# Optimization experiments

Measured on AMD Instinct MI355X. Metric: run time of the kernel, lower is better.

The kernel has to match this reference:

```python
import jax, jax.numpy as jnp
import numpy as np
import math

B, L, D = 8, 2048, 256
NUM_TYPES = 1
T_MAX = 200.0
SIGMA = 1.0


def setup_inputs() -> dict:
    key = jax.random.key(0)
    ks = jax.random.split(key, 12)
    event_type = jnp.ones((B, L), dtype=jnp.int64 if jax.config.jax_enable_x64 else jnp.int32)
    t = jax.random.uniform(ks[0], (B, L), dtype=jnp.float32) * T_MAX
    event_time = jnp.sort(t, axis=-1)
    s = 1.0 / math.sqrt(D)
    emb_weight = jax.random.normal(ks[1], (NUM_TYPES + 1, D), jnp.float32)
    emb_weight = emb_weight.at[0].set(0.0)  # padding_idx=0
    gate_w = jax.random.normal(ks[2], (2, D), jnp.float32) * s
    gate_b = jnp.zeros((2,), jnp.float32)
    ker_w = jax.random.normal(ks[3], (1, D), jnp.float32) * s
    ker_b = jnp.zeros((1,), jnp.float32)
    ln_gamma = jnp.ones((D,), jnp.float32)
    ln_beta = jnp.zeros((D,), jnp.float32)
    gen_input_w = jax.random.normal(ks[4], (D, D), jnp.float32) * s
    gen_noise_w = jax.random.normal(ks[5], (D, D), jnp.float32) * s
    gen_out_w = jax.random.normal(ks[6], (1, D), jnp.float32) * s
    gen_out_b = jnp.zeros((1,), jnp.float32)
    noise = jax.random.uniform(ks[7], (B, L, D), jnp.float32)  # torch.rand noise in Generator
    return dict(event_type=event_type, event_time=event_time, emb_weight=emb_weight,
                gate_w=gate_w, gate_b=gate_b, ker_w=ker_w, ker_b=ker_b,
                ln_gamma=ln_gamma, ln_beta=ln_beta, gen_input_w=gen_input_w,
                gen_noise_w=gen_noise_w, gen_out_w=gen_out_w, gen_out_b=gen_out_b,
                noise=noise)


def _softplus_beta(x, beta):
    return jax.nn.softplus(beta * x) / beta


def reference(event_type, event_time, emb_weight, gate_w, gate_b, ker_w, ker_b,
              ln_gamma, ln_beta, gen_input_w, gen_noise_w, gen_out_w, gen_out_b, noise):
    d_model = emb_weight.shape[-1]
    # ---- temporal positional encoding (this is `embedding`) ----
    pos_vec = jnp.power(10000.0, 2.0 * jnp.arange(d_model, dtype=jnp.float32) / d_model)
    t = event_time[:, :, None] / pos_vec                      # [B,L,D]
    idx = jnp.arange(d_model)
    temp_enc = jnp.where(idx % 2 == 0, jnp.sin(t), jnp.cos(t))
    # ---- type embedding ----
    te = emb_weight[event_type] * math.sqrt(d_model)          # [B,L,D]
    # ---- pairwise |t_i - t_j| ; xt[b,i,j]=t_i, xt_bar[b,i,j]=t_j ----
    dt = jnp.abs(event_time[:, :, None] - event_time[:, None, :])  # [B,L,L]
    # ---- squared exponential kernel: params depend only on row i (xd[b,i,j]=te[b,i]) ----
    ls = _softplus_beta(te @ ker_w.T + ker_b, 0.2)[..., 0]    # [B,L]
    scores_k = (SIGMA ** 2) * jnp.exp(-(dt ** 2) / (ls[:, :, None] ** 2))
    # ---- sigmoid gate ----
    p = jax.nn.sigmoid(te @ gate_w.T + gate_b)                # [B,L,2]
    l = p[..., 0][:, :, None]
    s = p[..., 1][:, :, None]
    gate = 1.0 + 0.5 * jnp.tanh((dt / T_MAX - l) / s)
    scores = scores_k * gate                                  # [B,L,L]
    # ---- causal mask: strictly-upper-triangle -> -1e10, then softmax ----
    causal = jnp.tril(jnp.ones((event_time.shape[1], event_time.shape[1]), jnp.bool_))
    scores = jnp.where(causal[None], scores, -1e10)
    attn = jax.nn.softmax(scores, axis=-1)
    # ---- hidden = attn @ temp_enc, layernorm ----
    hidden = jnp.einsum('bij,bjd->bid', attn, temp_enc)
    mu = hidden.mean(-1, keepdims=True)
    var = hidden.var(-1, keepdims=True)
    hidden = (hidden - mu) / jnp.sqrt(var + 1e-6) * ln_gamma + ln_beta
    # ---- Generator (dropout in eval = identity) ----
    h = jax.nn.relu(noise @ gen_noise_w.T + hidden @ gen_input_w.T)
    out = jax.nn.softplus(h @ gen_out_w.T + gen_out_b)[..., 0]  # [B,L]
    return out
```

## Files before the change

### kernel.cpp

```cpp
#include <hip/hip_runtime.h>
#include <hip/hip_bf16.h>

#define BD 8
#define LD 2048
#define DD 256

typedef unsigned short ushort_t;
typedef __attribute__((ext_vector_type(8))) short short8;
typedef __attribute__((ext_vector_type(4))) float floatx4;

__device__ __forceinline__ ushort_t f2bfu(float x) {
  __hip_bfloat16 h = __float2bfloat16(x);
  return *reinterpret_cast<ushort_t*>(&h);
}

__device__ __forceinline__ void dma16(const ushort_t* g, ushort_t* l) {
  __builtin_amdgcn_global_load_lds(
      (const __attribute__((address_space(1))) unsigned int*)g,
      (__attribute__((address_space(3))) unsigned int*)l,
      16, 0, 0);
}

__device__ __forceinline__ float sin_acc(float a) {
  float k = rintf(a * 0.15915494f);
  float r = __builtin_fmaf(-k, 6.2831855f, a);
  r = __builtin_fmaf(-k, -1.7484555e-7f, r);
  return __sinf(r);
}
__device__ __forceinline__ float cos_acc(float a) {
  float k = rintf(a * 0.15915494f);
  float r = __builtin_fmaf(-k, 6.2831855f, a);
  r = __builtin_fmaf(-k, -1.7484555e-7f, r);
  return __cosf(r);
}

__global__ __launch_bounds__(256) void k_dots(
    const float* __restrict__ embw, const float* __restrict__ gatew,
    const float* __restrict__ gateb, const float* __restrict__ kerw,
    const float* __restrict__ kerb, float* __restrict__ ptable)
{
  int d = threadIdx.x;
  int lane = d & 63, wvi = d >> 6;
  __shared__ float red[4][3];
  for (int ty = 0; ty < 2; ++ty) {
    float te = embw[ty * DD + d] * 16.0f;
    float p1 = te * kerw[d];
    float p2 = te * gatew[d];
    float p3 = te * gatew[DD + d];
    #pragma unroll
    for (int off = 32; off > 0; off >>= 1) {
      p1 += __shfl_xor(p1, off);
      p2 += __shfl_xor(p2, off);
      p3 += __shfl_xor(p3, off);
    }
    if (lane == 0) { red[wvi][0] = p1; red[wvi][1] = p2; red[wvi][2] = p3; }
    __syncthreads();
    if (d == 0) {
      float s1 = red[0][0] + red[1][0] + red[2][0] + red[3][0] + kerb[0];
      float s2 = red[0][1] + red[1][1] + red[2][1] + red[3][1] + gateb[0];
      float s3 = red[0][2] + red[1][2] + red[2][2] + red[3][2] + gateb[1];
      float z = 0.2f * s1;
      float sp = (z > 15.0f) ? z : log1pf(__expf(z));
      float ls = 5.0f * sp;
      ptable[ty * 4 + 0] = 1.0f / (ls * ls);
      ptable[ty * 4 + 1] = 1.0f / (1.0f + __expf(-s2));
      float s = 1.0f / (1.0f + __expf(-s3));
      ptable[ty * 4 + 2] = 1.0f / s;
    }
    __syncthreads();
  }
}

__global__ __launch_bounds__(256) void k_prep_enc(
    const float* __restrict__ etime, ushort_t* __restrict__ enc_bf)
{
  int bk = blockIdx.x;
  int tid = threadIdx.x;
  __shared__ float ts[32];
  if (tid < 32) ts[tid] = etime[(bk >> 6) * LD + (bk & 63) * 32 + tid];
  __syncthreads();
  uint4* dst = (uint4*)(enc_bf + (size_t)bk * 8192);
  const int jb = (tid & 3) * 8;
  #pragma unroll
  for (int jblk = 0; jblk < 4; ++jblk) {
    int d = jblk * 64 + (tid >> 2);
    float freq = __expf(-0.07195578416f * (float)d);
    unsigned int pk[4];
    #pragma unroll
    for (int p = 0; p < 4; ++p) {
      float a0 = ts[jb + 2 * p] * freq;
      float a1 = ts[jb + 2 * p + 1] * freq;
      float v0 = (d & 1) ? cos_acc(a0) : sin_acc(a0);
      float v1 = (d & 1) ? cos_acc(a1) : sin_acc(a1);
      pk[p] = (unsigned int)f2bfu(v0) | ((unsigned int)f2bfu(v1) << 16);
    }
    dst[jblk * 256 + tid] = make_uint4(pk[0], pk[1], pk[2], pk[3]);
  }
}

__global__ __launch_bounds__(256) void k_cast(
    const float* __restrict__ noise, const float* __restrict__ wn,
    const float* __restrict__ wi, ushort_t* __restrict__ noise_bf,
    ushort_t* __restrict__ wcat)
{
  int idx = blockIdx.x * 256 + threadIdx.x;
  if (idx < 1048576) {
    float4 f = ((const float4*)noise)[idx];
    ushort4 u;
    u.x = f2bfu(f.x); u.y = f2bfu(f.y); u.z = f2bfu(f.z); u.w = f2bfu(f.w);
    *(ushort4*)(noise_bf + (size_t)idx * 4) = u;
  } else {
    int p = idx - 1048576;
    int c = p >> 7;
    int k = (p & 127) * 4;
    const float* src = (k < 256) ? (wn + c * 256 + k) : (wi + c * 256 + (k - 256));
    float4 f = *(const float4*)src;
    ushort4 u;
    u.x = f2bfu(f.x); u.y = f2bfu(f.y); u.z = f2bfu(f.z); u.w = f2bfu(f.w);
    *(ushort4*)(wcat + (size_t)c * 512 + k) = u;
  }
}

__global__ __launch_bounds__(256, 4) void k_attn(
    const ushort_t* __restrict__ enc_bf, const float* __restrict__ etime,
    const int* __restrict__ etype, const float* __restrict__ ptable,
    const float* __restrict__ gamma, const float* __restrict__ beta,
    ushort_t* __restrict__ hidden_bf)
{
  __shared__ __align__(16) ushort_t stage[4][8192];
  const int tid = threadIdx.x;
  const int lane = tid & 63, wv = tid >> 6;
  const int bk = blockIdx.x;
  const int b = bk & 7;
  const int tl = 127 - (bk >> 3);
  const int base = b * LD;
  const int m = lane & 15, kg = lane >> 4;
  const int i = tl * 16 + m;
  const float ti = etime[base + i];
  const int ty = etype[base + i];
  const float il = ptable[ty * 4 + 0];
  const float ll = ptable[ty * 4 + 1];
  const float is2 = 2.0f * ptable[ty * 4 + 2];
  floatx4 acc[16];
  #pragma unroll
  for (int nt = 0; nt < 16; ++nt) acc[nt] = (floatx4){0.f, 0.f, 0.f, 0.f};
  const int nch = tl / 2 + 1;
  const ushort_t* __restrict__ encC = enc_bf + (size_t)(b * 64) * 8192;
  const int boff = m * 32 + kg * 8;
  ushort_t* mybuf = &stage[wv][0];
  for (int ch = wv; ch < nch; ch += 4) {
    const int j0 = ch * 32 + kg * 8;
    float4 tja = *(const float4*)(etime + base + j0);
    float4 tjb = *(const float4*)(etime + base + j0 + 4);
    __builtin_amdgcn_s_waitcnt(0xC07F);
    const ushort_t* gsrc = encC + (size_t)ch * 8192 + lane * 8;
    #pragma unroll
    for (int nt = 0; nt < 16; ++nt)
      dma16(gsrc + nt * 512, mybuf + nt * 512);
    float tj[8] = {tja.x, tja.y, tja.z, tja.w, tjb.x, tjb.y, tjb.z, tjb.w};
    short8 af;
    #pragma unroll
    for (int v = 0; v < 8; ++v) {
      float dt = fabsf(ti - tj[v]);
      float sk = __expf(-dt * dt * il);
      float rg = __builtin_amdgcn_rcpf(__expf((dt * 0.005f - ll) * is2) + 1.0f);
      float w = __expf(sk * (1.5f - rg));
      w = (j0 + v <= i) ? w : 0.0f;
      af[v] = (short)f2bfu(w);
    }
    __builtin_amdgcn_s_waitcnt(0x0F70);
    #pragma unroll
    for (int nt = 0; nt < 16; ++nt) {
      short8 bf = *(const short8*)(mybuf + nt * 512 + boff);
      acc[nt] = __builtin_amdgcn_mfma_f32_16x16x32_bf16(af, bf, acc[nt], 0, 0, 0);
    }
  }
  __syncthreads();
  floatx4* lds_acc = (floatx4*)&stage[0][0];
  if (wv != 0) {
    #pragma unroll
    for (int nt = 0; nt < 16; ++nt) lds_acc[(nt * 3 + (wv - 1)) * 64 + lane] = acc[nt];
  }
  __syncthreads();
  if (wv == 0) {
    #pragma unroll
    for (int nt = 0; nt < 16; ++nt) {
      acc[nt] += lds_acc[(nt * 3 + 0) * 64 + lane];
      acc[nt] += lds_acc[(nt * 3 + 1) * 64 + lane];
      acc[nt] += lds_acc[(nt * 3 + 2) * 64 + lane];
    }
    float gl[16], cl[16];
    #pragma unroll
    for (int nt = 0; nt < 16; ++nt) { gl[nt] = gamma[nt * 16 + m]; cl[nt] = beta[nt * 16 + m]; }
    const int q = lane >> 4;
    #pragma unroll
    for (int r = 0; r < 4; ++r) {
      float h[16];
      float sm = 0.0f, sq = 0.0f;
      #pragma unroll
      for (int nt = 0; nt < 16; ++nt) {
        h[nt] = acc[nt][r];
        sm += h[nt]; sq += h[nt] * h[nt];
      }
      #pragma unroll
      for (int off = 1; off < 16; off <<= 1) {
        sm += __shfl_xor(sm, off);
        sq += __shfl_xor(sq, off);
      }
      float mean = sm * (1.0f / 256.0f);
      float var = sq * (1.0f / 256.0f) - mean * mean;
      float rstd = rsqrtf(var + 1e-6f);
      const int row = q * 4 + r;
      ushort_t* dst = hidden_bf + ((size_t)(base + tl * 16 + row)) * DD + m;
      #pragma unroll
      for (int nt = 0; nt < 16; ++nt)
        dst[nt * 16] = f2bfu((h[nt] - mean) * rstd * gl[nt] + cl[nt]);
    }
  }
}

__global__ __launch_bounds__(256) void k_gen(
    const ushort_t* __restrict__ noise_bf, const ushort_t* __restrict__ hidden_bf,
    const ushort_t* __restrict__ wcat, const float* __restrict__ wout,
    const float* __restrict__ bout, float* __restrict__ out)
{
  __shared__ float pbuf[4][2][16];
  const int tid = threadIdx.x;
  const int lane = tid & 63, wv = tid >> 6;
  const int m = lane & 15, kg = lane >> 4;
  const int r0 = blockIdx.x * 32 + m;
  const ushort_t* __restrict__ an0 = noise_bf + (size_t)r0 * DD;
  const ushort_t* __restrict__ an1 = noise_bf + (size_t)(r0 + 16) * DD;
  const ushort_t* __restrict__ ah0 = hidden_bf + (size_t)r0 * DD;
  const ushort_t* __restrict__ ah1 = hidden_bf + (size_t)(r0 + 16) * DD;
  floatx4 acc[2][4];
  #pragma unroll
  for (int t = 0; t < 2; ++t)
    #pragma unroll
    for (int n = 0; n < 4; ++n) acc[t][n] = (floatx4){0.f, 0.f, 0.f, 0.f};
  const ushort_t* __restrict__ bbase = wcat + ((size_t)(wv * 4) * 16 + m) * 512 + kg * 8;
  #pragma unroll
  for (int ks = 0; ks < 16; ++ks) {
    const int koff = (ks & 7) * 32 + kg * 8;
    short8 a0 = *(const short8*)(((ks < 8) ? an0 : ah0) + koff);
    short8 a1 = *(const short8*)(((ks < 8) ? an1 : ah1) + koff);
    const ushort_t* bp = bbase + ks * 32;
    #pragma unroll
    for (int n = 0; n < 4; ++n) {
      short8 bf = *(const short8*)(bp + (size_t)n * 8192);
      acc[0][n] = __builtin_amdgcn_mfma_f32_16x16x32_bf16(a0, bf, acc[0][n], 0, 0, 0);
      acc[1][n] = __builtin_amdgcn_mfma_f32_16x16x32_bf16(a1, bf, acc[1][n], 0, 0, 0);
    }
  }
  float wo_l[4];
  #pragma unroll
  for (int n = 0; n < 4; ++n) wo_l[n] = wout[(wv * 4 + n) * 16 + m];
  #pragma unroll
  for (int t = 0; t < 2; ++t) {
    #pragma unroll
    for (int r4 = 0; r4 < 4; ++r4) {
      float p = 0.0f;
      #pragma unroll
      for (int n = 0; n < 4; ++n) p += fmaxf(acc[t][n][r4], 0.0f) * wo_l[n];
      #pragma unroll
      for (int off = 1; off < 16; off <<= 1) p += __shfl_xor(p, off);
      if (m == 0) pbuf[wv][t][kg * 4 + r4] = p;
    }
  }
  __syncthreads();
  if (tid < 32) {
    int t = tid >> 4, rr = tid & 15;
    float x = pbuf[0][t][rr] + pbuf[1][t][rr] + pbuf[2][t][rr] + pbuf[3][t][rr] + bout[0];
    float sp = (x > 15.0f) ? x : log1pf(__expf(x));
    out[blockIdx.x * 32 + t * 16 + rr] = sp;
  }
}

extern "C" void kernel_launch(void* const* d_in, const int* in_sizes, int n_in,
                              void* d_out, int out_size, void* d_ws, size_t ws_size,
                              hipStream_t stream) {
  const int*   etype = (const int*)d_in[0];
  const float* etime = (const float*)d_in[1];
  const float* embw  = (const float*)d_in[2];
  const float* gatew = (const float*)d_in[3];
  const float* gateb = (const float*)d_in[4];
  const float* kerw  = (const float*)d_in[5];
  const float* kerb  = (const float*)d_in[6];
  const float* gamma = (const float*)d_in[7];
  const float* beta  = (const float*)d_in[8];
  const float* wi    = (const float*)d_in[9];
  const float* wn    = (const float*)d_in[10];
  const float* wo    = (const float*)d_in[11];
  const float* bo    = (const float*)d_in[12];
  const float* noise = (const float*)d_in[13];
  float* out = (float*)d_out;

  char* w8 = (char*)d_ws;
  float* ptable       = (float*)(w8);
  ushort_t* enc_bf    = (ushort_t*)(w8 + 262144);
  ushort_t* hidden_bf = (ushort_t*)(w8 + 262144 + 8388608);
  ushort_t* noise_bf  = (ushort_t*)(w8 + 262144 + 2 * 8388608);
  ushort_t* wcat      = (ushort_t*)(w8 + 262144 + 3 * 8388608);

  k_dots<<<1, 256, 0, stream>>>(embw, gatew, gateb, kerw, kerb, ptable);
  k_prep_enc<<<512, 256, 0, stream>>>(etime, enc_bf);
  k_cast<<<4224, 256, 0, stream>>>(noise, wn, wi, noise_bf, wcat);
  k_attn<<<1024, 256, 0, stream>>>(enc_bf, etime, etype, ptable,
                                   gamma, beta, hidden_bf);
  k_gen<<<512, 256, 0, stream>>>(noise_bf, hidden_bf, wcat, wo, bo, out);
}
```

Measured before the change: 162.3 us.

## Merge prep kernels and restructure attention into two-tile blocks with shared double-buffered staging

Result: slower. 183.1 us (+12.8%).

```diff
diff --git a/kernel.cpp b/kernel.cpp
--- a/kernel.cpp
+++ b/kernel.cpp
@@ -34,90 +34,86 @@
   return __cosf(r);
 }
 
-__global__ __launch_bounds__(256) void k_dots(
+__global__ __launch_bounds__(256) void k_prep(
+    const int* __restrict__ etype, const float* __restrict__ etime,
     const float* __restrict__ embw, const float* __restrict__ gatew,
     const float* __restrict__ gateb, const float* __restrict__ kerw,
-    const float* __restrict__ kerb, float* __restrict__ ptable)
+    const float* __restrict__ kerb, const float* __restrict__ noise,
+    const float* __restrict__ wn, const float* __restrict__ wi,
+    ushort_t* __restrict__ enc_bf, ushort_t* __restrict__ noise_bf,
+    ushort_t* __restrict__ wcat, float* __restrict__ ptable)
 {
-  int d = threadIdx.x;
-  int lane = d & 63, wvi = d >> 6;
-  __shared__ float red[4][3];
-  for (int ty = 0; ty < 2; ++ty) {
-    float te = embw[ty * DD + d] * 16.0f;
-    float p1 = te * kerw[d];
-    float p2 = te * gatew[d];
-    float p3 = te * gatew[DD + d];
-    #pragma unroll
-    for (int off = 32; off > 0; off >>= 1) {
-      p1 += __shfl_xor(p1, off);
-      p2 += __shfl_xor(p2, off);
-      p3 += __shfl_xor(p3, off);
-    }
-    if (lane == 0) { red[wvi][0] = p1; red[wvi][1] = p2; red[wvi][2] = p3; }
+  const int bk = blockIdx.x;
+  const int tid = threadIdx.x;
+  if (bk < 4224) {
+    int idx = bk * 256 + tid;
+    if (idx < 1048576) {
+      float4 f = ((const float4*)noise)[idx];
+      ushort4 u;
+      u.x = f2bfu(f.x); u.y = f2bfu(f.y); u.z = f2bfu(f.z); u.w = f2bfu(f.w);
+      *(ushort4*)(noise_bf + (size_t)idx * 4) = u;
+    } else {
+      int p = idx - 1048576;
+      int c = p >> 7;
+      int k = (p & 127) * 4;
+      const float* src = (k < 256) ? (wn + c * 256 + k) : (wi + c * 256 + (k - 256));
+      float4 f = *(const float4*)src;
+      ushort4 u;
+      u.x = f2bfu(f.x); u.y = f2bfu(f.y); u.z = f2bfu(f.z); u.w = f2bfu(f.w);
+      *(ushort4*)(wcat + (size_t)c * 512 + k) = u;
+    }
+  } else if (bk < 4736) {
+    int ebk = bk - 4224;
+    __shared__ float ts[32];
+    if (tid < 32) ts[tid] = etime[(ebk >> 6) * LD + (ebk & 63) * 32 + tid];
     __syncthreads();
-    if (d == 0) {
-      float s1 = red[0][0] + red[1][0] + red[2][0] + red[3][0] + kerb[0];
-      float s2 = red[0][1] + red[1][1] + red[2][1] + red[3][1] + gateb[0];
-      float s3 = red[0][2] + red[1][2] + red[2][2] + red[3][2] + gateb[1];
-      float z = 0.2f * s1;
-      float sp = (z > 15.0f) ? z : log1pf(__expf(z));
-      float ls = 5.0f * sp;
-      ptable[ty * 4 + 0] = 1.0f / (ls * ls);
-      ptable[ty * 4 + 1] = 1.0f / (1.0f + __expf(-s2));
-      float s = 1.0f / (1.0f + __expf(-s3));
-      ptable[ty * 4 + 2] = 1.0f / s;
-    }
-    __syncthreads();
-  }
-}
-
-__global__ __launch_bounds__(256) void k_prep_enc(
-    const float* __restrict__ etime, ushort_t* __restrict__ enc_bf)
-{
-  int bk = blockIdx.x;
-  int tid = threadIdx.x;
-  __shared__ float ts[32];
-  if (tid < 32) ts[tid] = etime[(bk >> 6) * LD + (bk & 63) * 32 + tid];
-  __syncthreads();
-  uint4* dst = (uint4*)(enc_bf + (size_t)bk * 8192);
-  const int jb = (tid & 3) * 8;
-  #pragma unroll
-  for (int jblk = 0; jblk < 4; ++jblk) {
-    int d = jblk * 64 + (tid >> 2);
-    float freq = __expf(-0.07195578416f * (float)d);
-    unsigned int pk[4];
-    #pragma unroll
-    for (int p = 0; p < 4; ++p) {
-      float a0 = ts[jb + 2 * p] * freq;
-      float a1 = ts[jb + 2 * p + 1] * freq;
-      float v0 = (d & 1) ? cos_acc(a0) : sin_acc(a0);
-      float v1 = (d & 1) ? cos_acc(a1) : sin_acc(a1);
-      pk[p] = (unsigned int)f2bfu(v0) | ((unsigned int)f2bfu(v1) << 16);
-    }
-    dst[jblk * 256 + tid] = make_uint4(pk[0], pk[1], pk[2], pk[3]);
-  }
-}
-
-__global__ __launch_bounds__(256) void k_cast(
-    const float* __restrict__ noise, const float* __restrict__ wn,
-    const float* __restrict__ wi, ushort_t* __restrict__ noise_bf,
-    ushort_t* __restrict__ wcat)
-{
-  int idx = blockIdx.x * 256 + threadIdx.x;
-  if (idx < 1048576) {
-    float4 f = ((const float4*)noise)[idx];
-    ushort4 u;
-    u.x = f2bfu(f.x); u.y = f2bfu(f.y); u.z = f2bfu(f.z); u.w = f2bfu(f.w);
-    *(ushort4*)(noise_bf + (size_t)idx * 4) = u;
+    uint4* dst = (uint4*)(enc_bf + (size_t)ebk * 8192);
+    const int jb = (tid & 3) * 8;
+    #pragma unroll
+    for (int jblk = 0; jblk < 4; ++jblk) {
+      int d = jblk * 64 + (tid >> 2);
+      float freq = __expf(-0.07195578416f * (float)d);
+      unsigned int pk[4];
+      #pragma unroll
+      for (int p = 0; p < 4; ++p) {
+        float a0 = ts[jb + 2 * p] * freq;
+        float a1 = ts[jb + 2 * p + 1] * freq;
+        float v0 = (d & 1) ? cos_acc(a0) : sin_acc(a0);
+        float v1 = (d & 1) ? cos_acc(a1) : sin_acc(a1);
+        pk[p] = (unsigned int)f2bfu(v0) | ((unsigned int)f2bfu(v1) << 16);
+      }
+      dst[jblk * 256 + tid] = make_uint4(pk[0], pk[1], pk[2], pk[3]);
+    }
   } else {
-    int p = idx - 1048576;
-    int c = p >> 7;
-    int k = (p & 127) * 4;
-    const float* src = (k < 256) ? (wn + c * 256 + k) : (wi + c * 256 + (k - 256));
-    float4 f = *(const float4*)src;
-    ushort4 u;
-    u.x = f2bfu(f.x); u.y = f2bfu(f.y); u.z = f2bfu(f.z); u.w = f2bfu(f.w);
-    *(ushort4*)(wcat + (size_t)c * 512 + k) = u;
+    __shared__ float red[4][3];
+    int lane = tid & 63, wvi = tid >> 6;
+    for (int ty = 0; ty < 2; ++ty) {
+      float te = embw[ty * DD + tid] * 16.0f;
+      float p1 = te * kerw[tid];
+      float p2 = te * gatew[tid];
+      float p3 = te * gatew[DD + tid];
+      #pragma unroll
+      for (int off = 32; off > 0; off >>= 1) {
+        p1 += __shfl_xor(p1, off);
+        p2 += __shfl_xor(p2, off);
+        p3 += __shfl_xor(p3, off);
+      }
+      if (lane == 0) { red[wvi][0] = p1; red[wvi][1] = p2; red[wvi][2] = p3; }
+      __syncthreads();
+      if (tid == 0) {
+        float s1 = red[0][0] + red[1][0] + red[2][0] + red[3][0] + kerb[0];
+        float s2 = red[0][1] + red[1][1] + red[2][1] + red[3][1] + gateb[0];
+        float s3 = red[0][2] + red[1][2] + red[2][2] + red[3][2] + gateb[1];
+        float z = 0.2f * s1;
+        float sp = (z > 15.0f) ? z : log1pf(__expf(z));
+        float ls = 5.0f * sp;
+        ptable[ty * 4 + 0] = 1.0f / (ls * ls);
+        ptable[ty * 4 + 1] = 1.0f / (1.0f + __expf(-s2));
+        float s = 1.0f / (1.0f + __expf(-s3));
+        ptable[ty * 4 + 2] = 1.0f / s;
+      }
+      __syncthreads();
+    }
   }
 }
 
@@ -127,15 +123,17 @@
     const float* __restrict__ gamma, const float* __restrict__ beta,
     ushort_t* __restrict__ hidden_bf)
 {
-  __shared__ __align__(16) ushort_t stage[4][8192];
+  __shared__ __align__(16) ushort_t stage[2][8192];
   const int tid = threadIdx.x;
   const int lane = tid & 63, wv = tid >> 6;
   const int bk = blockIdx.x;
   const int b = bk & 7;
-  const int tl = 127 - (bk >> 3);
+  const int rb = 63 - (bk >> 3);
   const int base = b * LD;
   const int m = lane & 15, kg = lane >> 4;
-  const int i = tl * 16 + m;
+  const int tile = 2 * rb + (wv >> 1);
+  const int p = wv & 1;
+  const int i = tile * 16 + m;
   const float ti = etime[base + i];
   const int ty = etype[base + i];
   const float il = ptable[ty * 4 + 0];
@@ -144,51 +142,74 @@
   floatx4 acc[16];
   #pragma unroll
   for (int nt = 0; nt < 16; ++nt) acc[nt] = (floatx4){0.f, 0.f, 0.f, 0.f};
-  const int nch = tl / 2 + 1;
+  const int nch = rb + 1;
   const ushort_t* __restrict__ encC = enc_bf + (size_t)(b * 64) * 8192;
+  const int fr0 = wv * 4;
   const int boff = m * 32 + kg * 8;
-  ushort_t* mybuf = &stage[wv][0];
-  for (int ch = wv; ch < nch; ch += 4) {
-    const int j0 = ch * 32 + kg * 8;
-    float4 tja = *(const float4*)(etime + base + j0);
-    float4 tjb = *(const float4*)(etime + base + j0 + 4);
-    __builtin_amdgcn_s_waitcnt(0xC07F);
-    const ushort_t* gsrc = encC + (size_t)ch * 8192 + lane * 8;
-    #pragma unroll
-    for (int nt = 0; nt < 16; ++nt)
-      dma16(gsrc + nt * 512, mybuf + nt * 512);
-    float tj[8] = {tja.x, tja.y, tja.z, tja.w, tjb.x, tjb.y, tjb.z, tjb.w};
+  {
+    const ushort_t* g = encC + fr0 * 512 + lane * 8;
+    #pragma unroll
+    for (int q = 0; q < 4; ++q) dma16(g + q * 512, &stage[0][(fr0 + q) * 512]);
+  }
+  float tj[8];
+  if (p == 0) {
+    float4 a = *(const float4*)(etime + base + kg * 8);
+    float4 c = *(const float4*)(etime + base + kg * 8 + 4);
+    tj[0] = a.x; tj[1] = a.y; tj[2] = a.z; tj[3] = a.w;
+    tj[4] = c.x; tj[5] = c.y; tj[6] = c.z; tj[7] = c.w;
+  }
+  for (int ch = 0; ch < nch; ++ch) {
+    const int cur = ch & 1;
+    const bool mine = ((ch & 1) == p);
     short8 af;
-    #pragma unroll
-    for (int v = 0; v < 8; ++v) {
-      float dt = fabsf(ti - tj[v]);
-      float sk = __expf(-dt * dt * il);
-      float rg = __builtin_amdgcn_rcpf(__expf((dt * 0.005f - ll) * is2) + 1.0f);
-      float w = __expf(sk * (1.5f - rg));
-      w = (j0 + v <= i) ? w : 0.0f;
-      af[v] = (short)f2bfu(w);
-    }
-    __builtin_amdgcn_s_waitcnt(0x0F70);
-    #pragma unroll
-    for (int nt = 0; nt < 16; ++nt) {
-      short8 bf = *(const short8*)(mybuf + nt * 512 + boff);
-      acc[nt] = __builtin_amdgcn_mfma_f32_16x16x32_bf16(af, bf, acc[nt], 0, 0, 0);
+    if (mine) {
+      const int j0 = ch * 32 + kg * 8;
+      #pragma unroll
+      for (int v = 0; v < 8; ++v) {
+        float dt = ti - tj[v];
+        float sk = __expf(-dt * dt * il);
+        float rg = __builtin_amdgcn_rcpf(__expf((dt * 0.005f - ll) * is2) + 1.0f);
+        float w = __expf(sk * (1.5f - rg));
+        w = (j0 + v <= i) ? w : 0.0f;
+        af[v] = (short)f2bfu(w);
+      }
+    }
+    __syncthreads();
+    if (ch + 1 < nch) {
+      const ushort_t* g = encC + (size_t)(ch + 1) * 8192 + fr0 * 512 + lane * 8;
+      #pragma unroll
+      for (int q = 0; q < 4; ++q) dma16(g + q * 512, &stage[cur ^ 1][(fr0 + q) * 512]);
+      if (((ch + 1) & 1) == p) {
+        const int j0n = (ch + 1) * 32 + kg * 8;
+        float4 a = *(const float4*)(etime + base + j0n);
+        float4 c = *(const float4*)(etime + base + j0n + 4);
+        tj[0] = a.x; tj[1] = a.y; tj[2] = a.z; tj[3] = a.w;
+        tj[4] = c.x; tj[5] = c.y; tj[6] = c.z; tj[7] = c.w;
+      }
+    }
+    if (mine) {
+      #pragma unroll
+      for (int nt = 0; nt < 16; ++nt) {
+        short8 bf = *(const short8*)(&stage[cur][nt * 512 + boff]);
+        acc[nt] = __builtin_amdgcn_mfma_f32_16x16x32_bf16(af, bf, acc[nt], 0, 0, 0);
+      }
     }
   }
   __syncthreads();
-  floatx4* lds_acc = (floatx4*)&stage[0][0];
-  if (wv != 0) {
-    #pragma unroll
-    for (int nt = 0; nt < 16; ++nt) lds_acc[(nt * 3 + (wv - 1)) * 64 + lane] = acc[nt];
+  floatx4* reg0 = (floatx4*)&stage[0][0];
+  floatx4* reg1 = (floatx4*)&stage[1][0];
+  if (wv == 1) {
+    #pragma unroll
+    for (int nt = 0; nt < 16; ++nt) reg0[nt * 64 + lane] = acc[nt];
+  } else if (wv == 3) {
+    #pragma unroll
+    for (int nt = 0; nt < 16; ++nt) reg1[nt * 64 + lane] = acc[nt];
   }
   __syncthreads();
-  if (wv == 0) {
-    #pragma unroll
-    for (int nt = 0; nt < 16; ++nt) {
-      acc[nt] += lds_acc[(nt * 3 + 0) * 64 + lane];
-      acc[nt] += lds_acc[(nt * 3 + 1) * 64 + lane];
-      acc[nt] += lds_acc[(nt * 3 + 2) * 64 + lane];
-    }
+  if ((wv & 1) == 0) {
+    floatx4* reg = (wv == 0) ? reg0 : reg1;
+    #pragma unroll
+    for (int nt = 0; nt < 16; ++nt) acc[nt] += reg[nt * 64 + lane];
     float gl[16], cl[16];
     #pragma unroll
     for (int nt = 0; nt < 16; ++nt) { gl[nt] = gamma[nt * 16 + m]; cl[nt] = beta[nt * 16 + m]; }
@@ -211,7 +232,7 @@
       float var = sq * (1.0f / 256.0f) - mean * mean;
       float rstd = rsqrtf(var + 1e-6f);
       const int row = q * 4 + r;
-      ushort_t* dst = hidden_bf + ((size_t)(base + tl * 16 + row)) * DD + m;
+      ushort_t* dst = hidden_bf + ((size_t)(base + tile * 16 + row)) * DD + m;
       #pragma unroll
       for (int nt = 0; nt < 16; ++nt)
         dst[nt * 16] = f2bfu((h[nt] - mean) * rstd * gl[nt] + cl[nt]);
@@ -302,10 +323,9 @@
   ushort_t* noise_bf  = (ushort_t*)(w8 + 262144 + 2 * 8388608);
   ushort_t* wcat      = (ushort_t*)(w8 + 262144 + 3 * 8388608);
 
-  k_dots<<<1, 256, 0, stream>>>(embw, gatew, gateb, kerw, kerb, ptable);
-  k_prep_enc<<<512, 256, 0, stream>>>(etime, enc_bf);
-  k_cast<<<4224, 256, 0, stream>>>(noise, wn, wi, noise_bf, wcat);
-  k_attn<<<1024, 256, 0, stream>>>(enc_bf, etime, etype, ptable,
-                                   gamma, beta, hidden_bf);
+  k_prep<<<4737, 256, 0, stream>>>(etype, etime, embw, gatew, gateb, kerw, kerb,
+                                   noise, wn, wi, enc_bf, noise_bf, wcat, ptable);
+  k_attn<<<512, 256, 0, stream>>>(enc_bf, etime, etype, ptable,
+                                  gamma, beta, hidden_bf);
   k_gen<<<512, 256, 0, stream>>>(noise_bf, hidden_bf, wcat, wo, bo, out);
 }
```
